# Kernel tuning notes

Hardware: AMD Instinct MI355X
Metric: run time of the kernel (lower is better)

The kernel has to match this reference:

```python
import jax, jax.numpy as jnp
import numpy as np

H_DIM, W_DIM, D_MODEL = 128, 128, 1024
N_HEADS, HEAD_DIM = 16, 64


def setup_inputs() -> dict:
    key = jax.random.key(0)
    ks = jax.random.split(key, 8)
    s = D_MODEL ** -0.5
    return {
        "hidden_state": jax.random.normal(ks[0], (H_DIM, W_DIM, D_MODEL), jnp.float32),
        "attn_mask": jnp.zeros((1, 1, W_DIM, W_DIM), jnp.float32),
        "cos": jax.random.uniform(ks[1], (H_DIM, W_DIM, 1, HEAD_DIM), jnp.float32),
        "sin": jax.random.uniform(ks[2], (H_DIM, W_DIM, 1, HEAD_DIM), jnp.float32),
        "Wq": jax.random.normal(ks[3], (D_MODEL, N_HEADS * HEAD_DIM), jnp.float32) * s,
        "Wk": jax.random.normal(ks[4], (D_MODEL, N_HEADS * HEAD_DIM), jnp.float32) * s,
        "Wv": jax.random.normal(ks[5], (D_MODEL, N_HEADS * HEAD_DIM), jnp.float32) * s,
        "Wo": jax.random.normal(ks[6], (2 * D_MODEL, D_MODEL), jnp.float32) * s,
    }


def _rotate_half(x):
    x1, x2 = jnp.split(x, 2, axis=-1)
    return jnp.concatenate((-x2, x1), axis=-1)


def reference(hidden_state, attn_mask, cos, sin, Wq, Wk, Wv, Wo):
    h, w, d = hidden_state.shape
    Dh = cos.shape[-1]
    nH = d // Dh
    # projections (no bias) + RoPE on q/k
    q = (hidden_state @ Wq).reshape(h, w, nH, Dh)
    k = (hidden_state @ Wk).reshape(h, w, nH, Dh)
    v = (hidden_state @ Wv).reshape(h, w, nH, Dh)
    q = q * cos + _rotate_half(q) * sin
    k = k * cos + _rotate_half(k) * sin
    # NOTE: original divides by sqrt(hidden_size), not sqrt(head_dim)
    scale = jnp.sqrt(jnp.asarray(d, hidden_state.dtype))
    # ---- width attention: (h, w, nH, Dh) -> (h, nH, w, Dh) ----
    qx, kx, vx = (t.transpose(0, 2, 1, 3) for t in (q, k, v))
    sx = jnp.einsum('ahqd,ahkd->ahqk', qx, kx) / scale + attn_mask  # (h, nH, w, w)
    ow = jnp.einsum('ahqk,ahkd->ahqd', jax.nn.softmax(sx, axis=-1), vx)
    w_weights = ow.transpose(0, 2, 1, 3)  # (h, w, nH, Dh)
    # ---- height attention: (h, w, nH, Dh) -> (w, nH, h, Dh) ----
    qy, ky, vy = (t.transpose(1, 2, 0, 3) for t in (q, k, v))
    my = jnp.transpose(attn_mask, (2, 1, 0, 3))
    sy = jnp.einsum('ahqd,ahkd->ahqk', qy, ky) / scale + my  # (w, nH, h, h)
    oh = jnp.einsum('ahqk,ahkd->ahqd', jax.nn.softmax(sy, axis=-1), vy)
    h_weights = oh.transpose(2, 0, 1, 3)  # (h, w, nH, Dh)
    cat = jnp.concatenate([w_weights.reshape(h, w, d), h_weights.reshape(h, w, d)], axis=-1)
    return cat @ Wo
```

## Files before the change

### kernel.cpp

```cpp
#include <hip/hip_runtime.h>

typedef unsigned short u16;
typedef unsigned int   u32;
typedef __bf16 bf16;
typedef bf16  bf16x8 __attribute__((ext_vector_type(8)));
typedef float f32x4  __attribute__((ext_vector_type(4)));

__device__ __forceinline__ u16 bf16u(float f) {
    u32 x = __builtin_bit_cast(u32, f);
    x += 0x7fffu + ((x >> 16) & 1u);
    return (u16)(x >> 16);
}

__device__ __forceinline__ void gl_lds16(const void* g, void* l) {
    __builtin_amdgcn_global_load_lds(
        (const __attribute__((address_space(1))) u32*)g,
        (__attribute__((address_space(3))) u32*)l, 16, 0, 0);
}

__global__ __launch_bounds__(256) void cvt_x_kernel(const float4* __restrict__ in,
                                                    ushort4* __restrict__ out, int n4) {
    int i = blockIdx.x * 256 + threadIdx.x;
    if (i >= n4) return;
    float4 f = in[i];
    ushort4 o;
    o.x = bf16u(f.x); o.y = bf16u(f.y); o.z = bf16u(f.z); o.w = bf16u(f.w);
    out[i] = o;
}

__global__ __launch_bounds__(256) void transp_all(
    const float* __restrict__ Wq, const float* __restrict__ Wk,
    const float* __restrict__ Wv, const float* __restrict__ Wo,
    u16* __restrict__ WqkvT, u16* __restrict__ WoT)
{
    const int z = blockIdx.z;
    const float* W; u16* WT; int rows, cols;
    if (z < 3) {
        if (blockIdx.y >= 32) return;
        W = (z == 0) ? Wq : (z == 1) ? Wk : Wv;
        WT = WqkvT + (size_t)z * 1024 * 1024;
        rows = 1024; cols = 1024;
    } else {
        W = Wo; WT = WoT; rows = 2048; cols = 1024;
    }
    __shared__ float t[32][33];
    int bx = blockIdx.x * 32, by = blockIdx.y * 32;
    int x = threadIdx.x & 31, y = threadIdx.x >> 5;
#pragma unroll
    for (int i = 0; i < 32; i += 8)
        t[y + i][x] = W[(size_t)(by + y + i) * cols + bx + x];
    __syncthreads();
#pragma unroll
    for (int i = 0; i < 32; i += 8)
        WT[(size_t)(bx + y + i) * rows + by + x] = bf16u(t[x][y + i]);
}

#define BAR   __builtin_amdgcn_s_barrier()
#define VM0   asm volatile("s_waitcnt vmcnt(0)" ::: "memory")

__global__ __launch_bounds__(256, 2) void gemm_pp(
    const u16* __restrict__ A, const u16* __restrict__ BT, void* __restrict__ Cout,
    const float* __restrict__ cosp, const float* __restrict__ sinp,
    int M, int N, int K, int mode)
{
    __shared__ u16 Ld[4][8192];
    const int tid = threadIdx.x;
    const int wid = tid >> 6, lane = tid & 63;
    const int nx = gridDim.x;
    const int nwg = nx * gridDim.y;
    const int orig = blockIdx.y * nx + blockIdx.x;
    const int vid = (orig & 7) * (nwg >> 3) + (orig >> 3);
    const int m0 = (vid / nx) << 7, n0 = (vid % nx) << 7;
    const int wr = wid >> 1, wc = wid & 1;

    const int srow = tid >> 2;
    const int sg = (tid & 3) ^ ((srow >> 1) & 3);
    const u16* aS = A + (size_t)(m0 + srow) * K + (sg << 3);
    const u16* bS = BT + (size_t)(n0 + srow) * K + (sg << 3);
    const size_t h64K = (size_t)64 * K;
    const int wdb = wid << 9;
    const int nt = K >> 5;

#define STAGE(T) do { const int _b = (T) & 3; const size_t _ko = (size_t)(T) << 5; \
        gl_lds16(aS + _ko,        &Ld[_b][wdb]); \
        gl_lds16(aS + _ko + h64K, &Ld[_b][2048 + wdb]); \
        gl_lds16(bS + _ko,        &Ld[_b][4096 + wdb]); \
        gl_lds16(bS + _ko + h64K, &Ld[_b][6144 + wdb]); } while (0)

    const int phys = ((lane >> 4) ^ ((lane >> 1) & 3)) << 3;
    const int raw = ((wr << 6) + (lane & 15)) << 5;
    const int rbw = (((wc << 6) + (lane & 15)) << 5) + 4096;

    f32x4 acc[4][4] = {};

    STAGE(0); STAGE(1);
    VM0; BAR;

    for (int t = 0; t < nt; t += 2) {
        if (t + 2 < nt) STAGE(t + 2);
        if (t + 3 < nt) STAGE(t + 3);
        {
            const u16* Lb = &Ld[t & 3][0];
            bf16x8 af[4], bfr[4];
#pragma unroll
            for (int i = 0; i < 4; i++)
                af[i] = *(const bf16x8*)&Lb[raw + (i << 9) + phys];
#pragma unroll
            for (int i = 0; i < 4; i++)
                bfr[i] = *(const bf16x8*)&Lb[rbw + (i << 9) + phys];
            __builtin_amdgcn_s_setprio(1);
#pragma unroll
            for (int mi = 0; mi < 4; mi++)
#pragma unroll
                for (int ni = 0; ni < 4; ni++)
                    acc[mi][ni] = __builtin_amdgcn_mfma_f32_16x16x32_bf16(
                        af[mi], bfr[ni], acc[mi][ni], 0, 0, 0);
            __builtin_amdgcn_s_setprio(0);
        }
        {
            const u16* Lb = &Ld[(t + 1) & 3][0];
            bf16x8 af[4], bfr[4];
#pragma unroll
            for (int i = 0; i < 4; i++)
                af[i] = *(const bf16x8*)&Lb[raw + (i << 9) + phys];
#pragma unroll
            for (int i = 0; i < 4; i++)
                bfr[i] = *(const bf16x8*)&Lb[rbw + (i << 9) + phys];
            __builtin_amdgcn_s_setprio(1);
#pragma unroll
            for (int mi = 0; mi < 4; mi++)
#pragma unroll
                for (int ni = 0; ni < 4; ni++)
                    acc[mi][ni] = __builtin_amdgcn_mfma_f32_16x16x32_bf16(
                        af[mi], bfr[ni], acc[mi][ni], 0, 0, 0);
            __builtin_amdgcn_s_setprio(0);
        }
        VM0; BAR;
    }
#undef STAGE

    const int colbase = n0 + (wc << 6) + (lane & 15);
    if (mode == 2) {
        float* C = (float*)Cout;
#pragma unroll
        for (int mi = 0; mi < 4; mi++)
#pragma unroll
            for (int r = 0; r < 4; r++) {
                int m = m0 + (wr << 6) + (mi << 4) + ((lane >> 4) << 2) + r;
                float* row = C + (size_t)m * N + colbase;
#pragma unroll
                for (int ni = 0; ni < 4; ni++) row[ni << 4] = acc[mi][ni][r];
            }
    } else if (n0 < 2048) {
        u16* C = (u16*)Cout;
#pragma unroll
        for (int mi = 0; mi < 4; mi++)
#pragma unroll
            for (int r = 0; r < 4; r++) {
                int m = m0 + (wr << 6) + (mi << 4) + ((lane >> 4) << 2) + r;
                const float* cb = cosp + ((size_t)m << 6);
                const float* sb = sinp + ((size_t)m << 6);
                u16* row = C + (size_t)m * N + colbase;
#pragma unroll
                for (int ni = 0; ni < 4; ni++) {
                    int d = (ni << 4) + (lane & 15);
                    float c = cb[d], s = sb[d];
                    float v0 = acc[mi][ni][r];
                    float vr = acc[mi][ni ^ 2][r];
                    float o = fmaf(v0, c, (ni < 2 ? -vr : vr) * s);
                    row[ni << 4] = bf16u(o);
                }
            }
    } else {
        u16* C = (u16*)Cout;
#pragma unroll
        for (int mi = 0; mi < 4; mi++)
#pragma unroll
            for (int r = 0; r < 4; r++) {
                int m = m0 + (wr << 6) + (mi << 4) + ((lane >> 4) << 2) + r;
                u16* row = C + (size_t)m * N + colbase;
#pragma unroll
                for (int ni = 0; ni < 4; ni++) row[ni << 4] = bf16u(acc[mi][ni][r]);
            }
    }
}

__global__ __launch_bounds__(256) void axial_attn(
    const u16* __restrict__ qkv, const float* __restrict__ mask,
    u16* __restrict__ cat)
{
    __shared__ u16 Kl[128 * 64];
    __shared__ u16 VT[64 * 128];
    __shared__ u16 Pl[128 * 128];
    const int hmode = blockIdx.x >> 11;
    const int o2 = blockIdx.x & 2047;
    const int b = (o2 & 7) * 256 + (o2 >> 3);
    const int a = b >> 4, hd = b & 15;
    const int tid = threadIdx.x, wid = tid >> 6, lane = tid & 63;
    const int tmul = hmode ? 128 : 1;
    const int tadd = hmode ? a : (a << 7);
    const size_t hoff = (size_t)hd << 6;

#pragma unroll
    for (int c = 0; c < 4; c++) {
        int row = (wid << 5) + (c << 3) + (lane >> 3);
        int sc = (lane & 7) ^ (row & 7);
        gl_lds16(qkv + (size_t)(row * tmul + tadd) * 3072 + 1024 + hoff + (sc << 3),
                 &Kl[((wid << 5) + (c << 3)) << 6]);
    }
#pragma unroll
    for (int i = 0; i < 4; i++) {
        int cid = tid + (i << 8);
        int j = cid >> 3;
        int d0 = (cid & 7) << 3;
        uint4 raw = *(const uint4*)(qkv + (size_t)(j * tmul + tadd) * 3072 + 2048 + hoff + d0);
        const u16* e = (const u16*)&raw;
#pragma unroll
        for (int t = 0; t < 8; t++) {
            int d = d0 + t;
            VT[(d << 7) + (((j >> 3) ^ (d & 15)) << 3) + (j & 7)] = e[t];
        }
    }
    bf16x8 aq[2][2];
#pragma unroll
    for (int qt = 0; qt < 2; qt++)
#pragma unroll
        for (int ks = 0; ks < 2; ks++) {
            int row = (wid << 5) + (qt << 4) + (lane & 15);
            aq[qt][ks] = *(const bf16x8*)(qkv + (size_t)(row * tmul + tadd) * 3072 + hoff
                                          + (ks << 5) + ((lane >> 4) << 3));
        }
    __syncthreads();

    f32x4 S[2][8] = {};
#pragma unroll
    for (int kt = 0; kt < 8; kt++) {
        bf16x8 bk[2];
#pragma unroll
        for (int ks = 0; ks < 2; ks++) {
            int row = (kt << 4) + (lane & 15);
            int ch = ((ks << 2) + (lane >> 4)) ^ (row & 7);
            bk[ks] = *(const bf16x8*)&Kl[(row << 6) + (ch << 3)];
        }
#pragma unroll
        for (int qt = 0; qt < 2; qt++) {
            S[qt][kt] = __builtin_amdgcn_mfma_f32_16x16x32_bf16(aq[qt][0], bk[0], S[qt][kt], 0, 0, 0);
            S[qt][kt] = __builtin_amdgcn_mfma_f32_16x16x32_bf16(aq[qt][1], bk[1], S[qt][kt], 0, 0, 0);
        }
    }

    const float scale = 0.03125f;
#pragma unroll
    for (int qt = 0; qt < 2; qt++) {
#pragma unroll
        for (int r = 0; r < 4; r++) {
            int qrow = (wid << 5) + (qt << 4) + ((lane >> 4) << 2) + r;
            const float* mrow = mask + (hmode ? (a << 7) : (qrow << 7));
            float mx = -1e30f;
#pragma unroll
            for (int kt = 0; kt < 8; kt++) {
                float sv = fmaf(S[qt][kt][r], scale, mrow[(kt << 4) + (lane & 15)]);
                S[qt][kt][r] = sv;
                mx = fmaxf(mx, sv);
            }
            mx = fmaxf(mx, __shfl_xor(mx, 1));
            mx = fmaxf(mx, __shfl_xor(mx, 2));
            mx = fmaxf(mx, __shfl_xor(mx, 4));
            mx = fmaxf(mx, __shfl_xor(mx, 8));
            float sum = 0.f;
#pragma unroll
            for (int kt = 0; kt < 8; kt++) {
                float p = __expf(S[qt][kt][r] - mx);
                S[qt][kt][r] = p;
                sum += p;
            }
            sum += __shfl_xor(sum, 1);
            sum += __shfl_xor(sum, 2);
            sum += __shfl_xor(sum, 4);
            sum += __shfl_xor(sum, 8);
            float rinv = 1.0f / sum;
#pragma unroll
            for (int kt = 0; kt < 8; kt++) {
                int kcol = (kt << 4) + (lane & 15);
                int ch = (kcol >> 3) ^ (qrow & 15);
                Pl[(qrow << 7) + (ch << 3) + (kcol & 7)] = bf16u(S[qt][kt][r] * rinv);
            }
        }
    }
    __syncthreads();

    f32x4 O[4][2] = {};
#pragma unroll
    for (int ks = 0; ks < 4; ks++) {
        bf16x8 av[4], bp[2];
#pragma unroll
        for (int dt = 0; dt < 4; dt++) {
            int drow = (dt << 4) + (lane & 15);
            int ch = ((ks << 2) + (lane >> 4)) ^ (drow & 15);
            av[dt] = *(const bf16x8*)&VT[(drow << 7) + (ch << 3)];
        }
#pragma unroll
        for (int qt = 0; qt < 2; qt++) {
            int qrow = (wid << 5) + (qt << 4) + (lane & 15);
            int ch = ((ks << 2) + (lane >> 4)) ^ (qrow & 15);
            bp[qt] = *(const bf16x8*)&Pl[(qrow << 7) + (ch << 3)];
        }
#pragma unroll
        for (int dt = 0; dt < 4; dt++)
#pragma unroll
            for (int qt = 0; qt < 2; qt++)
                O[dt][qt] = __builtin_amdgcn_mfma_f32_16x16x32_bf16(av[dt], bp[qt], O[dt][qt], 0, 0, 0);
    }

    const int cbase = (hmode ? 1024 : 0) + (hd << 6);
#pragma unroll
    for (int dt = 0; dt < 4; dt++)
#pragma unroll
        for (int qt = 0; qt < 2; qt++) {
            int qrow = (wid << 5) + (qt << 4) + (lane & 15);
            int d0 = (dt << 4) + ((lane >> 4) << 2);
            size_t base = ((size_t)(qrow * tmul + tadd) << 11) + cbase + d0;
            ushort4 pk;
            pk.x = bf16u(O[dt][qt][0]);
            pk.y = bf16u(O[dt][qt][1]);
            pk.z = bf16u(O[dt][qt][2]);
            pk.w = bf16u(O[dt][qt][3]);
            *(ushort4*)(cat + base) = pk;
        }
}

extern "C" void kernel_launch(void* const* d_in, const int* in_sizes, int n_in,
                              void* d_out, int out_size, void* d_ws, size_t ws_size,
                              hipStream_t stream)
{
    (void)in_sizes; (void)n_in; (void)out_size; (void)ws_size;
    const float* hidden = (const float*)d_in[0];
    const float* mask   = (const float*)d_in[1];
    const float* cosp   = (const float*)d_in[2];
    const float* sinp   = (const float*)d_in[3];
    const float* Wq     = (const float*)d_in[4];
    const float* Wk     = (const float*)d_in[5];
    const float* Wv     = (const float*)d_in[6];
    const float* Wo     = (const float*)d_in[7];

    char* ws = (char*)d_ws;
    u16* Xb    = (u16*)(ws);
    u16* WqkvT = (u16*)(ws + 33554432);
    u16* cat   = (u16*)(ws);
    u16* WoT   = (u16*)(ws + 67108864);
    u16* qkvb  = (u16*)(ws + 71303168);

    cvt_x_kernel<<<16384, 256, 0, stream>>>((const float4*)hidden, (ushort4*)Xb, 4194304);
    transp_all<<<dim3(32, 64, 4), 256, 0, stream>>>(Wq, Wk, Wv, Wo, WqkvT, WoT);

    gemm_pp<<<dim3(24, 128), 256, 0, stream>>>(Xb, WqkvT, qkvb, cosp, sinp, 16384, 3072, 1024, 1);

    axial_attn<<<4096, 256, 0, stream>>>(qkvb, mask, cat);

    gemm_pp<<<dim3(8, 128), 256, 0, stream>>>(cat, WoT, d_out, nullptr, nullptr, 16384, 1024, 2048, 2);
}
```

Baseline: 331.1 us.

## Merge prep kernels and use 256x256 triple-buffered GEMM for output projection

Folds the fp32-to-bf16 conversion of the hidden state into the weight transpose kernel as an extra grid slice, removing one launch. Adds a new 512-thread GEMM with 256x256 tiles and a three-stage LDS pipeline, and uses it for the output projection. The larger tile raises data reuse per workgroup but cuts the grid to 256 workgroups, which may underfill the device and adds register pressure from 128 accumulators per thread.

```diff
diff --git a/kernel.cpp b/kernel.cpp
--- a/kernel.cpp
+++ b/kernel.cpp
@@ -18,22 +18,26 @@
         (__attribute__((address_space(3))) u32*)l, 16, 0, 0);
 }
 
-__global__ __launch_bounds__(256) void cvt_x_kernel(const float4* __restrict__ in,
-                                                    ushort4* __restrict__ out, int n4) {
-    int i = blockIdx.x * 256 + threadIdx.x;
-    if (i >= n4) return;
-    float4 f = in[i];
-    ushort4 o;
-    o.x = bf16u(f.x); o.y = bf16u(f.y); o.z = bf16u(f.z); o.w = bf16u(f.w);
-    out[i] = o;
-}
-
-__global__ __launch_bounds__(256) void transp_all(
+__global__ __launch_bounds__(256) void prep_all(
+    const float* __restrict__ hidden, ushort4* __restrict__ Xb,
     const float* __restrict__ Wq, const float* __restrict__ Wk,
     const float* __restrict__ Wv, const float* __restrict__ Wo,
     u16* __restrict__ WqkvT, u16* __restrict__ WoT)
 {
     const int z = blockIdx.z;
+    if (z == 4) {
+        const float4* in = (const float4*)hidden;
+        int b = blockIdx.y * 32 + blockIdx.x;
+#pragma unroll
+        for (int it = 0; it < 8; it++) {
+            int i = (b << 11) + (it << 8) + threadIdx.x;
+            float4 f = in[i];
+            ushort4 o;
+            o.x = bf16u(f.x); o.y = bf16u(f.y); o.z = bf16u(f.z); o.w = bf16u(f.w);
+            Xb[i] = o;
+        }
+        return;
+    }
     const float* W; u16* WT; int rows, cols;
     if (z < 3) {
         if (blockIdx.y >= 32) return;
@@ -56,6 +60,8 @@
 }
 
 #define BAR   __builtin_amdgcn_s_barrier()
+#define SB0   __builtin_amdgcn_sched_barrier(0)
+#define VM4   asm volatile("s_waitcnt vmcnt(4)" ::: "memory")
 #define VM0   asm volatile("s_waitcnt vmcnt(0)" ::: "memory")
 
 __global__ __launch_bounds__(256, 2) void gemm_pp(
@@ -178,6 +184,119 @@
 #pragma unroll
             for (int r = 0; r < 4; r++) {
                 int m = m0 + (wr << 6) + (mi << 4) + ((lane >> 4) << 2) + r;
+                u16* row = C + (size_t)m * N + colbase;
+#pragma unroll
+                for (int ni = 0; ni < 4; ni++) row[ni << 4] = bf16u(acc[mi][ni][r]);
+            }
+    }
+}
+
+__global__ __launch_bounds__(512, 2) void gemm_fat(
+    const u16* __restrict__ A, const u16* __restrict__ BT, void* __restrict__ Cout,
+    const float* __restrict__ cosp, const float* __restrict__ sinp,
+    int M, int N, int K, int mode)
+{
+    __shared__ u16 Ld[3][16384];
+    const int tid = threadIdx.x;
+    const int wid = tid >> 6, lane = tid & 63;
+    const int nx = gridDim.x;
+    const int nwg = nx * gridDim.y;
+    const int orig = blockIdx.y * nx + blockIdx.x;
+    const int vid = (orig & 7) * (nwg >> 3) + (orig >> 3);
+    const int m0 = (vid / nx) << 8, n0 = (vid % nx) << 8;
+    const int wr = wid >> 2, wc = wid & 3;
+
+    const int srow = tid >> 2;
+    const int sl = (tid & 3) ^ ((srow >> 1) & 3);
+    const u16* aS0 = A + (size_t)(m0 + srow) * K + (sl << 3);
+    const u16* aS1 = aS0 + (size_t)128 * K;
+    const u16* bS0 = BT + (size_t)(n0 + srow) * K + (sl << 3);
+    const u16* bS1 = bS0 + (size_t)128 * K;
+    const int wdb = wid << 9;
+    const int nt = K >> 5;
+
+#define STAGE(T, B_) do { if ((T) < nt) { size_t _ko = (size_t)(T) << 5; \
+        gl_lds16(aS0 + _ko, &Ld[B_][wdb]); \
+        gl_lds16(aS1 + _ko, &Ld[B_][4096 + wdb]); \
+        gl_lds16(bS0 + _ko, &Ld[B_][8192 + wdb]); \
+        gl_lds16(bS1 + _ko, &Ld[B_][12288 + wdb]); } } while (0)
+
+    const int phys = ((lane >> 4) ^ ((lane >> 1) & 3)) << 3;
+    const int raw = ((wr << 7) + (lane & 15)) << 5;
+    const int rbw = (((wc << 6) + (lane & 15)) << 5) + 8192;
+
+    f32x4 acc[8][4] = {};
+
+    STAGE(0, 0); STAGE(1, 1);
+    VM4;
+    BAR; SB0;
+
+    int b = 0, bs = 2;
+    for (int t = 0; t < nt; ++t) {
+        const u16* Lb = &Ld[b][0];
+        bf16x8 fa[8], fb[4];
+#pragma unroll
+        for (int mi = 0; mi < 8; mi++)
+            fa[mi] = *(const bf16x8*)&Lb[raw + (mi << 9) + phys];
+#pragma unroll
+        for (int ni = 0; ni < 4; ni++)
+            fb[ni] = *(const bf16x8*)&Lb[rbw + (ni << 9) + phys];
+        STAGE(t + 2, bs);
+        BAR;
+        __builtin_amdgcn_s_setprio(1);
+#pragma unroll
+        for (int mi = 0; mi < 8; mi++)
+#pragma unroll
+            for (int ni = 0; ni < 4; ni++)
+                acc[mi][ni] = __builtin_amdgcn_mfma_f32_16x16x32_bf16(
+                    fa[mi], fb[ni], acc[mi][ni], 0, 0, 0);
+        __builtin_amdgcn_s_setprio(0);
+        if (t + 2 < nt) { VM4; } else { VM0; }
+        BAR; SB0;
+        b = (b == 2) ? 0 : b + 1;
+        bs = (bs == 2) ? 0 : bs + 1;
+    }
+#undef STAGE
+
+    const int colbase = n0 + (wc << 6) + (lane & 15);
+    if (mode == 2) {
+        float* C = (float*)Cout;
+#pragma unroll
+        for (int mi = 0; mi < 8; mi++)
+#pragma unroll
+            for (int r = 0; r < 4; r++) {
+                int m = m0 + (wr << 7) + (mi << 4) + ((lane >> 4) << 2) + r;
+                float* row = C + (size_t)m * N + colbase;
+#pragma unroll
+                for (int ni = 0; ni < 4; ni++) row[ni << 4] = acc[mi][ni][r];
+            }
+    } else if (n0 < 2048) {
+        u16* C = (u16*)Cout;
+#pragma unroll
+        for (int mi = 0; mi < 8; mi++)
+#pragma unroll
+            for (int r = 0; r < 4; r++) {
+                int m = m0 + (wr << 7) + (mi << 4) + ((lane >> 4) << 2) + r;
+                const float* cb = cosp + ((size_t)m << 6);
+                const float* sb = sinp + ((size_t)m << 6);
+                u16* row = C + (size_t)m * N + colbase;
+#pragma unroll
+                for (int ni = 0; ni < 4; ni++) {
+                    int d = (ni << 4) + (lane & 15);
+                    float c = cb[d], s = sb[d];
+                    float v0 = acc[mi][ni][r];
+                    float vr = acc[mi][ni ^ 2][r];
+                    float o = fmaf(v0, c, (ni < 2 ? -vr : vr) * s);
+                    row[ni << 4] = bf16u(o);
+                }
+            }
+    } else {
+        u16* C = (u16*)Cout;
+#pragma unroll
+        for (int mi = 0; mi < 8; mi++)
+#pragma unroll
+            for (int r = 0; r < 4; r++) {
+                int m = m0 + (wr << 7) + (mi << 4) + ((lane >> 4) << 2) + r;
                 u16* row = C + (size_t)m * N + colbase;
 #pragma unroll
                 for (int ni = 0; ni < 4; ni++) row[ni << 4] = bf16u(acc[mi][ni][r]);
@@ -350,12 +469,12 @@
     u16* WoT   = (u16*)(ws + 67108864);
     u16* qkvb  = (u16*)(ws + 71303168);
 
-    cvt_x_kernel<<<16384, 256, 0, stream>>>((const float4*)hidden, (ushort4*)Xb, 4194304);
-    transp_all<<<dim3(32, 64, 4), 256, 0, stream>>>(Wq, Wk, Wv, Wo, WqkvT, WoT);
+    prep_all<<<dim3(32, 64, 5), 256, 0, stream>>>(hidden, (ushort4*)Xb,
+                                                  Wq, Wk, Wv, Wo, WqkvT, WoT);
 
     gemm_pp<<<dim3(24, 128), 256, 0, stream>>>(Xb, WqkvT, qkvb, cosp, sinp, 16384, 3072, 1024, 1);
 
     axial_attn<<<4096, 256, 0, stream>>>(qkvb, mask, cat);
 
-    gemm_pp<<<dim3(8, 128), 256, 0, stream>>>(cat, WoT, d_out, nullptr, nullptr, 16384, 1024, 2048, 2);
-}
+    gemm_fat<<<dim3(4, 64), 512, 0, stream>>>(cat, WoT, d_out, nullptr, nullptr, 16384, 1024, 2048, 2);
+}
```

After: 322.8 us. 1.03x faster.
